# Kernel optimization log

Hardware: AMD Instinct MI355X
Metric: run time of the kernel (lower is better)

## Reference

```python
import jax, jax.numpy as jnp
import numpy as np

N_E = 1024
E_DIM = 64
BETA = 0.25


def setup_inputs() -> dict:
    key = jax.random.key(0)
    k_z, k_c = jax.random.split(key)
    z = jax.random.normal(k_z, (64, E_DIM, 32, 32), dtype=jnp.float32)  # [B, e_dim, H, W]
    # Codebook initialized uniform(-1/n_e, 1/n_e) as in the torch module
    codebook = jax.random.uniform(k_c, (N_E, E_DIM), dtype=jnp.float32,
                                  minval=-1.0 / N_E, maxval=1.0 / N_E)
    return {"z": z, "codebook": codebook}


def reference(z, codebook):
    beta = BETA
    n_e, e_dim = codebook.shape
    # [B, e_dim, H, W] -> [B, H, W, e_dim]
    z_nhwc = jnp.transpose(z, (0, 2, 3, 1))
    zf = z_nhwc.reshape(-1, e_dim)  # [N, e_dim]
    # Squared Euclidean distances: ||z||^2 + ||e||^2 - 2 z.e  -> [N, n_e]
    d = (jnp.sum(zf * zf, axis=1, keepdims=True)
         + jnp.sum(codebook * codebook, axis=1)
         - 2.0 * jnp.matmul(zf, codebook.T))
    min_encoding_indices = jnp.argmin(d, axis=1)[:, None]  # [N, 1]
    min_encodings = jax.nn.one_hot(min_encoding_indices[:, 0], n_e, dtype=zf.dtype)  # [N, n_e]
    # Gather codebook rows via one-hot matmul (same math as torch version)
    z_q = jnp.matmul(min_encodings, codebook).reshape(z_nhwc.shape)  # [B,H,W,e_dim]
    sg = jax.lax.stop_gradient
    loss = (jnp.mean((sg(z_nhwc) - z_q) ** 2)
            + beta * jnp.mean((z_nhwc - sg(z_q)) ** 2))
    # Straight-through estimator
    z_q = z_nhwc + sg(z_q - z_nhwc)
    z_q = jnp.transpose(z_q, (0, 3, 1, 2))  # back to [B, e_dim, H, W]
    return (loss, z_q, min_encodings, min_encoding_indices)
```

## Files before the change

kernel.cpp:

```cpp
#include <hip/hip_runtime.h>

#define N_ROWS 65536
#define NE 1024
#define ED 64
#define ERR_GAP 8e-5f

static const size_t OFF_ZQ = 1;
static const size_t OFF_ME = 1 + 4194304;
static const size_t OFF_IDX = OFF_ME + (size_t)N_ROWS * NE;
#define ME_FLOATS ((size_t)N_ROWS * NE)

#define SC_CBF  0

typedef __attribute__((ext_vector_type(8))) short short8v;
typedef __attribute__((ext_vector_type(4))) float f32x4;

__device__ __forceinline__ unsigned bf16_rne(float v) {
  unsigned u = __float_as_uint(v);
  return (u + 0x7FFFu + ((u >> 16) & 1u)) >> 16;
}

__device__ __forceinline__ void gld16(const void* g, void* l) {
  __builtin_amdgcn_global_load_lds(
      (const __attribute__((address_space(1))) void*)g,
      (__attribute__((address_space(3))) void*)l, 16, 0, 0);
}

__global__ __launch_bounds__(256) void k_e2cb(const float* __restrict__ cb,
                                              float* __restrict__ e2,
                                              short* __restrict__ cbfrag) {
  const int tid = blockIdx.x * 256 + threadIdx.x;
  const int ct = tid >> 6, lane = tid & 63;
  const int col = ct * 16 + (lane & 15);
  const int k0 = (lane >> 4) * 8;
  const float* __restrict__ ep = cb + (size_t)col * ED + k0;
  short* __restrict__ o = cbfrag + (size_t)ct * 2048 + lane * 8;
  #pragma unroll
  for (int ks = 0; ks < 2; ++ks) {
    short h[8], lo[8];
    #pragma unroll
    for (int i = 0; i < 8; ++i) {
      const float v = ep[ks * 32 + i];
      const unsigned hb = bf16_rne(v);
      const float res = v - __uint_as_float(hb << 16);
      h[i] = (short)hb; lo[i] = (short)bf16_rne(res);
    }
    *(short8v*)(o + (size_t)(0 * 2 + ks) * 512) = *(short8v*)h;
    *(short8v*)(o + (size_t)(1 * 2 + ks) * 512) = *(short8v*)lo;
  }
  if (threadIdx.x < 64) {
    const int j = blockIdx.x * 64 + threadIdx.x;
    const float* __restrict__ e = cb + (size_t)j * ED;
    float r[8];
    #pragma unroll
    for (int i = 0; i < 8; ++i) {
      float v = e[i]; float q = v * v;
      asm volatile("" : "+v"(q)); r[i] = q;
    }
    #pragma unroll
    for (int k = 1; k < 8; ++k)
      #pragma unroll
      for (int i = 0; i < 8; ++i) {
        float v = e[8 * k + i]; float q = v * v;
        asm volatile("" : "+v"(q)); r[i] += q;
      }
    e2[j] = ((r[0] + r[1]) + (r[2] + r[3])) + ((r[4] + r[5]) + (r[6] + r[7]));
  }
}

__global__ __launch_bounds__(256, 4) void k_distX(const float* __restrict__ z,
    const float* __restrict__ cb, const short* __restrict__ cbfrag,
    const float* __restrict__ e2g, float* __restrict__ idxf) {
  __shared__ float4 smem4[2320];
  short* lBs = (short*)smem4;
  float* e2l = (float*)(smem4 + 2048);
  float* z2l = (float*)(smem4 + 2304);
  float (*lzf)[65] = (float(*)[65])smem4;
  int* candL = (int*)smem4;
  int* nfl   = (int*)smem4 + 512;

  const int t = threadIdx.x, w = t >> 6, lane = t & 63;
  const int row0 = blockIdx.x * 64;

  gld16(e2g + w * 256 + lane * 4, e2l + w * 256);

  const int rl = w * 16 + (lane & 15);
  const int n0 = row0 + rl;
  const int bb = n0 >> 10, hw = n0 & 1023;
  const float* __restrict__ zp = z + (size_t)bb * 65536 + hw;
  const int k0 = (lane >> 4) * 8;
  #pragma unroll
  for (int ks = 0; ks < 2; ++ks)
    #pragma unroll
    for (int i = 0; i < 8; ++i)
      lzf[ks * 32 + k0 + i][rl] = zp[(size_t)(ks * 32 + k0 + i) << 10];
  __syncthreads();

  short8v a[2][2];
  #pragma unroll
  for (int ks = 0; ks < 2; ++ks) {
    short h[8], lo[8];
    #pragma unroll
    for (int i = 0; i < 8; ++i) {
      const float v = lzf[ks * 32 + k0 + i][rl];
      const unsigned hb = bf16_rne(v);
      const float res = v - __uint_as_float(hb << 16);
      h[i] = (short)hb; lo[i] = (short)bf16_rne(res);
    }
    a[0][ks] = *(short8v*)h;
    a[1][ks] = *(short8v*)lo;
  }
  if (t < 64) {
    float r[8];
    #pragma unroll
    for (int i = 0; i < 8; ++i) {
      const float v = lzf[i][t];
      float q = v * v; asm volatile("" : "+v"(q)); r[i] = q;
    }
    #pragma unroll
    for (int k = 1; k < 8; ++k)
      #pragma unroll
      for (int i = 0; i < 8; ++i) {
        const float v = lzf[8 * k + i][t];
        float q = v * v; asm volatile("" : "+v"(q)); r[i] += q;
      }
    z2l[t] = ((r[0] + r[1]) + (r[2] + r[3])) + ((r[4] + r[5]) + (r[6] + r[7]));
  }
  __syncthreads();

  #pragma unroll
  for (int i = 0; i < 4; ++i) {
    const int s = w * 4 + i;
    gld16(cbfrag + s * 512 + lane * 8, lBs + s * 512);
  }
  float z2r[4];
  #pragma unroll
  for (int reg = 0; reg < 4; ++reg)
    z2r[reg] = z2l[w * 16 + (lane >> 4) * 4 + reg];
  float Tm1[4], Tm2[4], Tm3[4]; int Tb1[4], Tb2[4];
  #pragma unroll
  for (int reg = 0; reg < 4; ++reg) {
    Tm1[reg] = 1e30f; Tm2[reg] = 1e30f; Tm3[reg] = 1e30f;
    Tb1[reg] = 0; Tb2[reg] = 0;
  }
  __syncthreads();

  int buf = 0;
  for (int c = 0; c < 16; ++c) {
    if (c < 15) {
      #pragma unroll
      for (int i = 0; i < 4; ++i) {
        const int s = w * 4 + i;
        gld16(cbfrag + (size_t)(c + 1) * 8192 + s * 512 + lane * 8,
              lBs + (buf ^ 1) * 8192 + s * 512);
      }
    }
    #pragma unroll 1
    for (int ctl = 0; ctl < 4; ++ctl) {
      short8v bfr[2][2];
      #pragma unroll
      for (int hl = 0; hl < 2; ++hl)
        #pragma unroll
        for (int ks = 0; ks < 2; ++ks)
          bfr[hl][ks] = *(const short8v*)(lBs + buf * 8192 +
              (ctl * 4 + hl * 2 + ks) * 512 + lane * 8);

      f32x4 acc = (f32x4)(0.0f);
      #pragma unroll
      for (int p = 0; p < 3; ++p) {
        const int pa = (p == 2) ? 1 : 0;
        const int pb = (p == 1) ? 1 : 0;
        #pragma unroll
        for (int ks = 0; ks < 2; ++ks)
          acc = __builtin_amdgcn_mfma_f32_16x16x32_bf16(a[pa][ks], bfr[pb][ks], acc, 0, 0, 0);
      }
      const int j = c * 64 + ctl * 16 + (lane & 15);
      const float e2v = e2l[j];
      #pragma unroll
      for (int reg = 0; reg < 4; ++reg) {
        const float dd = (z2r[reg] + e2v) - 2.0f * acc[reg];
        if (dd < Tm1[reg]) {
          Tm3[reg] = Tm2[reg]; Tm2[reg] = Tm1[reg]; Tb2[reg] = Tb1[reg];
          Tm1[reg] = dd; Tb1[reg] = j;
        } else if (dd < Tm2[reg]) {
          Tm3[reg] = Tm2[reg]; Tm2[reg] = dd; Tb2[reg] = j;
        } else if (dd < Tm3[reg]) {
          Tm3[reg] = dd;
        }
      }
    }
    __syncthreads();
    buf ^= 1;
  }

  #pragma unroll
  for (int reg = 0; reg < 4; ++reg) {
    float rm = Tm1[reg]; int ri = Tb1[reg];
    #pragma unroll
    for (int off = 1; off < 16; off <<= 1) {
      const float om = __shfl_xor(rm, off, 64);
      const int   oi = __shfl_xor(ri, off, 64);
      if (om < rm || (om == rm && oi < ri)) { rm = om; ri = oi; }
    }
    const float thr = rm + ERR_GAP;
    const bool c1 = (Tm1[reg] <= thr);
    const bool c2 = (Tm2[reg] <= thr);
    const bool c3 = (Tm3[reg] <= thr);
    const unsigned long long b1 = __ballot(c1);
    const unsigned long long b2 = __ballot(c2);
    const unsigned long long b3 = __ballot(c3);
    const int grp = lane >> 4;
    const unsigned m1m = (unsigned)((b1 >> (grp * 16)) & 0xFFFFull);
    const unsigned m2m = (unsigned)((b2 >> (grp * 16)) & 0xFFFFull);
    const unsigned m3m = (unsigned)((b3 >> (grp * 16)) & 0xFFFFull);
    const int n1 = __popc(m1m);
    const int ncand = n1 + __popc(m2m);
    const bool ovf = (m3m != 0u) || (ncand > 8);
    const int rowLocal = w * 16 + grp * 4 + reg;
    if (!ovf) {
      const unsigned below = (1u << (lane & 15)) - 1u;
      if (c1) candL[rowLocal * 8 + __popc(m1m & below)] = Tb1[reg];
      if (c2) candL[rowLocal * 8 + n1 + __popc(m2m & below)] = Tb2[reg];
    }
    if ((lane & 15) == 0) {
      const bool wrf = ovf || (ncand >= 2);
      nfl[rowLocal] = ovf ? 999 : (ncand >= 2 ? ncand : 0);
      if (!wrf) idxf[row0 + rowLocal] = (float)ri;
    }
  }
  __syncthreads();

  #pragma unroll 1
  for (int r = 0; r < 16; ++r) {
    const int rowLocal = w * 16 + r;
    const int fn = nfl[rowLocal];
    if (fn == 0) continue;
    const int n = row0 + rowLocal;
    const int b2 = n >> 10, hw2 = n & 1023;
    const float zv = z[(size_t)b2 * 65536 + ((size_t)lane << 10) + hw2];
    const float z2v = z2l[rowLocal];
    if (fn != 999) {
      const int ci = candL[rowLocal * 8 + (lane < fn ? lane : 0)];
      const float* __restrict__ e = cb + (size_t)ci * ED;
      float acl = 0.f;
      #pragma unroll 8
      for (int k = 0; k < ED; ++k)
        acl = fmaf(__shfl(zv, k, 64), e[k], acl);
      float d = (z2v + e2l[ci]) - 2.0f * acl;
      int bi = ci;
      if (lane >= fn) { d = 1e30f; bi = 0x7FFFFFFF; }
      #pragma unroll
      for (int off = 1; off < 8; off <<= 1) {
        const float om = __shfl_xor(d, off, 64);
        const int   oi = __shfl_xor(bi, off, 64);
        if (om < d || (om == d && oi < bi)) { d = om; bi = oi; }
      }
      if (lane == 0) idxf[n] = (float)bi;
    } else {
      float bm = 1e30f; int bi = 0;
      #pragma unroll 1
      for (int q = 0; q < 16; ++q) {
        const int j = lane * 16 + q;
        const float4* __restrict__ e4 = (const float4*)(cb + (size_t)j * ED);
        float acl = 0.f;
        #pragma unroll
        for (int p = 0; p < 16; ++p) {
          const float4 ee = e4[p];
          acl = fmaf(__shfl(zv, 4 * p + 0, 64), ee.x, acl);
          acl = fmaf(__shfl(zv, 4 * p + 1, 64), ee.y, acl);
          acl = fmaf(__shfl(zv, 4 * p + 2, 64), ee.z, acl);
          acl = fmaf(__shfl(zv, 4 * p + 3, 64), ee.w, acl);
        }
        const float d = (z2v + e2l[j]) - 2.0f * acl;
        if (d < bm) { bm = d; bi = j; }
      }
      #pragma unroll
      for (int off = 1; off < 64; off <<= 1) {
        const float om = __shfl_xor(bm, off, 64);
        const int   oi = __shfl_xor(bi, off, 64);
        if (om < bm || (om == bm && oi < bi)) { bm = om; bi = oi; }
      }
      if (lane == 0) idxf[n] = (float)bi;
    }
  }
}

__global__ __launch_bounds__(256) void k_zq(const float* __restrict__ z,
    const float* __restrict__ cb, const float* __restrict__ idxf,
    float* __restrict__ zq, float* __restrict__ partial) {
  float s = 0.f;
  #pragma unroll 1
  for (int it = 0; it < 8; ++it) {
    const int o = (it * 2048 + blockIdx.x) * 256 + threadIdx.x;
    const int b = o >> 16;
    const int d = (o >> 10) & 63;
    const int hw = o & 1023;
    const int n = (b << 10) + hw;
    const int idx = (int)idxf[n];
    const float v = cb[(size_t)idx * ED + d];
    zq[o] = v;
    const float diff = z[o] - v;
    s = fmaf(diff, diff, s);
  }
  #pragma unroll
  for (int off = 32; off > 0; off >>= 1) s += __shfl_xor(s, off, 64);
  __shared__ float sh[4];
  if ((threadIdx.x & 63) == 0) sh[threadIdx.x >> 6] = s;
  __syncthreads();
  if (threadIdx.x == 0)
    partial[blockIdx.x] = (sh[0] + sh[1]) + (sh[2] + sh[3]);
}

__global__ __launch_bounds__(256) void k_onehot(const float* __restrict__ idxf,
    const float* __restrict__ partial, float* __restrict__ me,
    float* __restrict__ out0) {
  __shared__ int idxL[32];
  const int t = threadIdx.x;
  const int n0 = blockIdx.x * 32;
  if (t < 32) idxL[t] = (int)idxf[n0 + t];
  __syncthreads();
  float* __restrict__ base = me + (size_t)n0 * 1024;
  float4* __restrict__ p4 = (float4*)(base + 3);
  #pragma unroll 1
  for (int s = t; s < 8191; s += 256) {
    const int f0 = 3 + 4 * s;
    const int row = f0 >> 10;
    const int col0 = f0 & 1023;
    float4 v;
    if (col0 <= 1020) {
      const int idx = idxL[row];
      v.x = (col0 == idx)     ? 1.0f : 0.0f;
      v.y = (col0 + 1 == idx) ? 1.0f : 0.0f;
      v.z = (col0 + 2 == idx) ? 1.0f : 0.0f;
      v.w = (col0 + 3 == idx) ? 1.0f : 0.0f;
    } else {
      v.x = (idxL[row] == 1023)    ? 1.0f : 0.0f;
      v.y = (idxL[row + 1] == 0)   ? 1.0f : 0.0f;
      v.z = (idxL[row + 1] == 1)   ? 1.0f : 0.0f;
      v.w = (idxL[row + 1] == 2)   ? 1.0f : 0.0f;
    }
    p4[s] = v;
  }
  if (t == 0) {
    base[0] = (idxL[0] == 0) ? 1.0f : 0.0f;
    base[1] = (idxL[0] == 1) ? 1.0f : 0.0f;
    base[2] = (idxL[0] == 2) ? 1.0f : 0.0f;
    base[32767] = (idxL[31] == 1023) ? 1.0f : 0.0f;
  }
  if (blockIdx.x == 0) {
    double sd = 0.0;
    #pragma unroll
    for (int k = 0; k < 8; ++k) sd += (double)partial[t + (k << 8)];
    #pragma unroll
    for (int off = 32; off > 0; off >>= 1) sd += __shfl_xor(sd, off, 64);
    __shared__ double shd[4];
    if ((t & 63) == 0) shd[t >> 6] = sd;
    __syncthreads();
    if (t == 0)
      out0[0] = (float)(1.25 * ((shd[0] + shd[1]) + (shd[2] + shd[3])) / 4194304.0);
  }
}

extern "C" void kernel_launch(void* const* d_in, const int* in_sizes, int n_in,
                              void* d_out, int out_size, void* d_ws, size_t ws_size,
                              hipStream_t stream) {
  const float* z  = (const float*)d_in[0];
  const float* cb = (const float*)d_in[1];
  float* out  = (float*)d_out;
  float* zq   = out + OFF_ZQ;
  float* me   = out + OFF_ME;
  float* idxf = out + OFF_IDX;
  float* sbase = out + 4;
  short* cbfrag = (short*)(sbase + SC_CBF);
  float* e2      = (float*)((char*)d_ws + 16);
  float* partial = (float*)((char*)d_ws + 4112);

  k_e2cb<<<16, 256, 0, stream>>>(cb, e2, cbfrag);
  k_distX<<<1024, 256, 0, stream>>>(z, cb, cbfrag, e2, idxf);
  k_zq<<<2048, 256, 0, stream>>>(z, cb, idxf, zq, partial);
  k_onehot<<<2048, 256, 0, stream>>>(idxf, partial, me, out);
}
```

Measured before the change: 164.4 us.

## Overlap one-hot zero-fill with distance kernel and scatter ones in zq kernel

Extra blocks in the distance kernel zero-fill the 256MB one-hot matrix while the other blocks compute argmin. The zq kernel then writes a single 1.0 per row, and the final loss reduction moves into it through a last-block atomic counter. This removes the separate one-hot kernel, which had to wait for the indices before writing. The cost is that the fill blocks compete with the compute blocks for the GPU, and the ones depend on kernel ordering for correctness.

```diff
diff --git a/kernel.cpp b/kernel.cpp
--- a/kernel.cpp
+++ b/kernel.cpp
@@ -28,7 +28,9 @@
 
 __global__ __launch_bounds__(256) void k_e2cb(const float* __restrict__ cb,
                                               float* __restrict__ e2,
-                                              short* __restrict__ cbfrag) {
+                                              short* __restrict__ cbfrag,
+                                              int* __restrict__ cnt) {
+  if (blockIdx.x == 0 && threadIdx.x == 0) *cnt = 0;
   const int tid = blockIdx.x * 256 + threadIdx.x;
   const int ct = tid >> 6, lane = tid & 63;
   const int col = ct * 16 + (lane & 15);
@@ -68,10 +70,24 @@
   }
 }
 
-__global__ __launch_bounds__(256, 4) void k_distX(const float* __restrict__ z,
+__global__ __launch_bounds__(256, 4) void k_distfill(const float* __restrict__ z,
     const float* __restrict__ cb, const short* __restrict__ cbfrag,
-    const float* __restrict__ e2g, float* __restrict__ idxf) {
+    const float* __restrict__ e2g, float* __restrict__ idxf,
+    float* __restrict__ me) {
   __shared__ float4 smem4[2320];
+  if (blockIdx.x >= 1024) {
+    const size_t n4 = (ME_FLOATS - 3) >> 2;
+    float4* __restrict__ p4 = reinterpret_cast<float4*>(me + 3);
+    const size_t stride = (size_t)2048 * 256;
+    const float4 zero4 = make_float4(0.f, 0.f, 0.f, 0.f);
+    for (size_t i = (size_t)(blockIdx.x - 1024) * 256 + threadIdx.x; i < n4; i += stride)
+      p4[i] = zero4;
+    if (blockIdx.x == 1024 && threadIdx.x == 0) {
+      me[0] = 0.f; me[1] = 0.f; me[2] = 0.f;
+      me[ME_FLOATS - 1] = 0.f;
+    }
+    return;
+  }
   short* lBs = (short*)smem4;
   float* e2l = (float*)(smem4 + 2048);
   float* z2l = (float*)(smem4 + 2304);
@@ -285,9 +301,12 @@
   }
 }
 
-__global__ __launch_bounds__(256) void k_zq(const float* __restrict__ z,
+__global__ __launch_bounds__(256) void k_zqhot(const float* __restrict__ z,
     const float* __restrict__ cb, const float* __restrict__ idxf,
-    float* __restrict__ zq, float* __restrict__ partial) {
+    float* __restrict__ zq, float* __restrict__ partial, float* __restrict__ me,
+    int* __restrict__ cnt, float* __restrict__ out0) {
+  __shared__ float sh[4];
+  __shared__ int isLast;
   float s = 0.f;
   #pragma unroll 1
   for (int it = 0; it < 8; ++it) {
@@ -299,55 +318,24 @@
     const int idx = (int)idxf[n];
     const float v = cb[(size_t)idx * ED + d];
     zq[o] = v;
+    if (d == 0) me[(size_t)n * NE + idx] = 1.0f;
     const float diff = z[o] - v;
     s = fmaf(diff, diff, s);
   }
   #pragma unroll
   for (int off = 32; off > 0; off >>= 1) s += __shfl_xor(s, off, 64);
-  __shared__ float sh[4];
   if ((threadIdx.x & 63) == 0) sh[threadIdx.x >> 6] = s;
   __syncthreads();
-  if (threadIdx.x == 0)
+  if (threadIdx.x == 0) {
     partial[blockIdx.x] = (sh[0] + sh[1]) + (sh[2] + sh[3]);
-}
-
-__global__ __launch_bounds__(256) void k_onehot(const float* __restrict__ idxf,
-    const float* __restrict__ partial, float* __restrict__ me,
-    float* __restrict__ out0) {
-  __shared__ int idxL[32];
-  const int t = threadIdx.x;
-  const int n0 = blockIdx.x * 32;
-  if (t < 32) idxL[t] = (int)idxf[n0 + t];
-  __syncthreads();
-  float* __restrict__ base = me + (size_t)n0 * 1024;
-  float4* __restrict__ p4 = (float4*)(base + 3);
-  #pragma unroll 1
-  for (int s = t; s < 8191; s += 256) {
-    const int f0 = 3 + 4 * s;
-    const int row = f0 >> 10;
-    const int col0 = f0 & 1023;
-    float4 v;
-    if (col0 <= 1020) {
-      const int idx = idxL[row];
-      v.x = (col0 == idx)     ? 1.0f : 0.0f;
-      v.y = (col0 + 1 == idx) ? 1.0f : 0.0f;
-      v.z = (col0 + 2 == idx) ? 1.0f : 0.0f;
-      v.w = (col0 + 3 == idx) ? 1.0f : 0.0f;
-    } else {
-      v.x = (idxL[row] == 1023)    ? 1.0f : 0.0f;
-      v.y = (idxL[row + 1] == 0)   ? 1.0f : 0.0f;
-      v.z = (idxL[row + 1] == 1)   ? 1.0f : 0.0f;
-      v.w = (idxL[row + 1] == 2)   ? 1.0f : 0.0f;
-    }
-    p4[s] = v;
-  }
-  if (t == 0) {
-    base[0] = (idxL[0] == 0) ? 1.0f : 0.0f;
-    base[1] = (idxL[0] == 1) ? 1.0f : 0.0f;
-    base[2] = (idxL[0] == 2) ? 1.0f : 0.0f;
-    base[32767] = (idxL[31] == 1023) ? 1.0f : 0.0f;
-  }
-  if (blockIdx.x == 0) {
+    __threadfence();
+    const int old = atomicAdd(cnt, 1);
+    isLast = (old == (int)gridDim.x - 1) ? 1 : 0;
+  }
+  __syncthreads();
+  if (isLast) {
+    __threadfence();
+    const int t = threadIdx.x;
     double sd = 0.0;
     #pragma unroll
     for (int k = 0; k < 8; ++k) sd += (double)partial[t + (k << 8)];
@@ -372,11 +360,11 @@
   float* idxf = out + OFF_IDX;
   float* sbase = out + 4;
   short* cbfrag = (short*)(sbase + SC_CBF);
+  int*   cnt     = (int*)((char*)d_ws + 8);
   float* e2      = (float*)((char*)d_ws + 16);
   float* partial = (float*)((char*)d_ws + 4112);
 
-  k_e2cb<<<16, 256, 0, stream>>>(cb, e2, cbfrag);
-  k_distX<<<1024, 256, 0, stream>>>(z, cb, cbfrag, e2, idxf);
-  k_zq<<<2048, 256, 0, stream>>>(z, cb, idxf, zq, partial);
-  k_onehot<<<2048, 256, 0, stream>>>(idxf, partial, me, out);
-}
+  k_e2cb<<<16, 256, 0, stream>>>(cb, e2, cbfrag, cnt);
+  k_distfill<<<3072, 256, 0, stream>>>(z, cb, cbfrag, e2, idxf, me);
+  k_zqhot<<<2048, 256, 0, stream>>>(z, cb, idxf, zq, partial, me, cnt, out);
+}
```

Result: slower. 209.8 us (+27.6%).
